# Performance work log

Measured on AMD Instinct MI355X. Metric: run time of the kernel, lower is better.

The kernel has to match this reference:

```python
import jax, jax.numpy as jnp
import numpy as np

N_NODES = 100000
N_EDGES = 3200000
N_GRAPHS = 256
DIMS = [11, 200, 200, 200, 200, 200]  # acfg_init_dims + cfg_filters
CONCAT = sum(DIMS[1:])  # 1000


def setup_inputs() -> dict:
    key = jax.random.key(0)
    ks = jax.random.split(key, 32)
    d = {}
    d["x"] = jax.random.normal(ks[0], (N_NODES, DIMS[0]), jnp.float32)
    d["edge_index"] = jax.random.randint(ks[1], (2, N_EDGES), 0, N_NODES)
    d["batch"] = jnp.sort(jax.random.randint(ks[2], (N_NODES,), 0, N_GRAPHS))
    ki = 3
    # SAGEConv params: lin_l (neighbors, with bias) + lin_r (root, no bias)
    for i in range(5):
        fi, fo = DIMS[i], DIMS[i + 1]
        s = 1.0 / np.sqrt(fi)
        d[f"Wl{i+1}"] = jax.random.uniform(ks[ki], (fo, fi), jnp.float32, -s, s); ki += 1
        d[f"bl{i+1}"] = jnp.zeros((fo,), jnp.float32)
        d[f"Wr{i+1}"] = jax.random.uniform(ks[ki], (fo, fi), jnp.float32, -s, s); ki += 1
    # projection head 1000 -> 500 -> 250 -> 1
    for j, (fi, fo) in enumerate([(CONCAT, CONCAT // 2), (CONCAT // 2, CONCAT // 4), (CONCAT // 4, 1)]):
        s = 1.0 / np.sqrt(fi)
        d[f"pw{j+1}"] = jax.random.uniform(ks[ki], (fo, fi), jnp.float32, -s, s); ki += 1
        d[f"pb{j+1}"] = jnp.zeros((fo,), jnp.float32)
    return d


def reference(x, edge_index, batch,
              Wl1, bl1, Wr1, Wl2, bl2, Wr2, Wl3, bl3, Wr3,
              Wl4, bl4, Wr4, Wl5, bl5, Wr5,
              pw1, pb1, pw2, pb2, pw3, pb3):
    src, dst = edge_index[0], edge_index[1]
    # in-degree for mean aggregation (computed once, reused by all layers)
    deg = jax.ops.segment_sum(jnp.ones((src.shape[0],), x.dtype), dst, N_NODES)
    inv_deg = (1.0 / jnp.maximum(deg, 1.0))[:, None]

    def sage(h, Wl, bl, Wr):
        agg = jax.ops.segment_sum(h[src], dst, N_NODES) * inv_deg  # mean of neighbor feats
        return agg @ Wl.T + bl + h @ Wr.T

    layers = [(Wl1, bl1, Wr1), (Wl2, bl2, Wr2), (Wl3, bl3, Wr3), (Wl4, bl4, Wr4), (Wl5, bl5, Wr5)]
    h = x
    outs = []
    for Wl, bl, Wr in layers:
        h = jax.nn.relu(sage(h, Wl, bl, Wr))
        outs.append(h)
    hc = jnp.concatenate(outs, axis=1)  # [N, 1000]

    # global_mean_pool over graph ids
    cnt = jax.ops.segment_sum(jnp.ones((x.shape[0],), x.dtype), batch, N_GRAPHS)
    g = jax.ops.segment_sum(hc, batch, N_GRAPHS) / jnp.maximum(cnt, 1.0)[:, None]

    # dropout is identity in eval mode (functional.dropout with training=False)
    g = g @ pw1.T + pb1
    g = g @ pw2.T + pb2
    g = g @ pw3.T + pb3  # [num_graphs, 1]
    return jax.nn.sigmoid(g).squeeze(1)
```

## Files before the change

kernel.cpp:

```cpp
#include <hip/hip_runtime.h>
#include <math.h>

typedef __attribute__((ext_vector_type(4))) float floatx4;
typedef __attribute__((ext_vector_type(2))) float floatx2;

#define ROWP 256
#define R4   16
#define NT 14
#define NTC 13
#define KS 7
#define PACK_BYTES (NT*KS*64*8)
#define PACK1_BYTES (NT*64*8)
#define STAGE_BYTES (NTC*KS*64*8)
#define BSHIFT 6
#define EPB 4096
#define MAXBUCK 1600

__device__ __forceinline__ unsigned short f2bf(float f){
    union { float f; unsigned u; } v; v.f = f;
    unsigned r = v.u + 0x7FFF + ((v.u >> 16) & 1);
    return (unsigned short)(r >> 16);
}
__device__ __forceinline__ unsigned pk4_fp8(float a, float b, float c, float d){
    int w = __builtin_amdgcn_cvt_pk_fp8_f32(a, b, 0, false);
    w = __builtin_amdgcn_cvt_pk_fp8_f32(c, d, w, true);
    return (unsigned)w;
}
__device__ __forceinline__ unsigned char b1_fp8(float a){
    int w = __builtin_amdgcn_cvt_pk_fp8_f32(a, a, 0, false);
    return (unsigned char)(w & 0xFF);
}


__global__ __launch_bounds__(256) void k_bin_hist(
    const int* __restrict__ dst, int* __restrict__ hist, int E, int nbuck)
{
    __shared__ int lh[MAXBUCK];
    for (int i = threadIdx.x; i < nbuck; i += 256) lh[i] = 0;
    __syncthreads();
    int base = blockIdx.x * EPB;
    #pragma unroll
    for (int k = 0; k < EPB / 256; ++k){
        int e = base + k * 256 + threadIdx.x;
        if (e < E) atomicAdd(&lh[dst[e] >> BSHIFT], 1);
    }
    __syncthreads();
    for (int i = threadIdx.x; i < nbuck; i += 256)
        hist[(size_t)blockIdx.x * nbuck + i] = lh[i];
}

__global__ __launch_bounds__(256) void k_col_scan(
    int* __restrict__ hist, int* __restrict__ T, int nblk, int nbuck)
{
    __shared__ int part[4][64];
    int w = threadIdx.x >> 6, l = threadIdx.x & 63;
    int b = blockIdx.x * 64 + l;
    int chunk = (nblk + 3) >> 2;
    int j0 = w * chunk, j1 = j0 + chunk; if (j1 > nblk) j1 = nblk;
    int s = 0;
    if (b < nbuck)
        for (int j = j0; j < j1; ++j) s += hist[(size_t)j * nbuck + b];
    part[w][l] = s;
    __syncthreads();
    if (b < nbuck){
        int run = 0;
        for (int w2 = 0; w2 < w; ++w2) run += part[w2][l];
        for (int j = j0; j < j1; ++j){
            int v = hist[(size_t)j * nbuck + b];
            hist[(size_t)j * nbuck + b] = run;
            run += v;
        }
        if (w == 3) T[b] = part[0][l] + part[1][l] + part[2][l] + part[3][l];
    }
}

__global__ __launch_bounds__(256) void k_scan_t(
    const int* __restrict__ T, int* __restrict__ tbase, int nbuck)
{
    __shared__ int ts[256];
    int t = threadIdx.x;
    int v[8]; int s = 0;
    int base = t * 8;
    #pragma unroll
    for (int k = 0; k < 8; ++k){
        int idx = base + k;
        v[k] = (idx < nbuck) ? T[idx] : 0;
        s += v[k];
    }
    ts[t] = s; __syncthreads();
    #pragma unroll
    for (int off = 1; off < 256; off <<= 1){
        int p = (t >= off) ? ts[t - off] : 0;
        __syncthreads();
        ts[t] += p;
        __syncthreads();
    }
    int run = ts[t] - s;
    #pragma unroll
    for (int k = 0; k < 8; ++k){
        int idx = base + k;
        if (idx < nbuck) tbase[idx] = run;
        run += v[k];
    }
    if (t == 255) tbase[nbuck] = ts[255];
}

__global__ __launch_bounds__(256) void k_bin_scatter(
    const int* __restrict__ src, const int* __restrict__ dst,
    const int* __restrict__ off, const int* __restrict__ tbase,
    unsigned* __restrict__ pairs, int E, int nbuck)
{
    __shared__ int lbase[MAXBUCK];
    __shared__ int lc[MAXBUCK];
    for (int i = threadIdx.x; i < nbuck; i += 256){
        lbase[i] = off[(size_t)blockIdx.x * nbuck + i] + tbase[i];
        lc[i] = 0;
    }
    __syncthreads();
    int base = blockIdx.x * EPB;
    #pragma unroll
    for (int k = 0; k < EPB / 256; ++k){
        int e = base + k * 256 + threadIdx.x;
        if (e < E){
            int d = dst[e];
            int b = d >> BSHIFT;
            int r = atomicAdd(&lc[b], 1);
            pairs[lbase[b] + r] = ((unsigned)(d & 63) << 26) | (unsigned)src[e];
        }
    }
}

__global__ __launch_bounds__(256) void k_bucket_deg(
    const unsigned* __restrict__ pairs, const int* __restrict__ tbase,
    int* __restrict__ deg, float* __restrict__ inv_deg, int N)
{
    __shared__ int ld[64];
    int b = blockIdx.x;
    if (threadIdx.x < 64) ld[threadIdx.x] = 0;
    __syncthreads();
    int pb = tbase[b], pe = tbase[b + 1];
    for (int e = pb + threadIdx.x; e < pe; e += 256)
        atomicAdd(&ld[pairs[e] >> 26], 1);
    __syncthreads();
    if (threadIdx.x < 64){
        int node = (b << BSHIFT) + threadIdx.x;
        if (node < N){
            int d = ld[threadIdx.x];
            deg[node] = d;
            inv_deg[node] = 1.0f / fmaxf((float)d, 1.0f);
        }
    }
}

__global__ __launch_bounds__(256) void k_place(
    const unsigned* __restrict__ pairs, const int* __restrict__ tbase,
    const int* __restrict__ row_ptr, int* __restrict__ srcs, int N)
{
    __shared__ int lrp[64];
    __shared__ int lcur[64];
    int b = blockIdx.x;
    if (threadIdx.x < 64){
        int node = (b << BSHIFT) + threadIdx.x;
        lrp[threadIdx.x] = (node < N) ? row_ptr[node] : 0;
        lcur[threadIdx.x] = 0;
    }
    __syncthreads();
    int pb = tbase[b], pe = tbase[b + 1];
    for (int e = pb + threadIdx.x; e < pe; e += 256){
        unsigned pr = pairs[e];
        int li = pr >> 26;
        int r = atomicAdd(&lcur[li], 1);
        srcs[lrp[li] + r] = (int)(pr & 0x03FFFFFFu);
    }
}


__global__ void k_scan_sums(const int* __restrict__ deg, int* __restrict__ csum, int N){
    __shared__ int sd[256];
    int base = blockIdx.x * 1024;
    int s = 0;
    for (int i = threadIdx.x; i < 1024; i += 256){
        int idx = base + i;
        s += (idx < N) ? deg[idx] : 0;
    }
    sd[threadIdx.x] = s; __syncthreads();
    for (int off = 128; off > 0; off >>= 1){
        if (threadIdx.x < off) sd[threadIdx.x] += sd[threadIdx.x + off];
        __syncthreads();
    }
    if (threadIdx.x == 0) csum[blockIdx.x] = sd[0];
}

__global__ void k_scan_apply(const int* __restrict__ deg, const int* __restrict__ csum,
                             int* __restrict__ row_ptr, int N, int E, int nchunks){
    __shared__ int ts[256];
    __shared__ int base_s;
    int partial = 0;
    for (int j = threadIdx.x; j < nchunks; j += 256)
        if (j < (int)blockIdx.x) partial += csum[j];
    ts[threadIdx.x] = partial; __syncthreads();
    for (int off = 128; off > 0; off >>= 1){
        if (threadIdx.x < off) ts[threadIdx.x] += ts[threadIdx.x + off];
        __syncthreads();
    }
    if (threadIdx.x == 0) base_s = ts[0];
    __syncthreads();
    int blk_base = base_s;
    __syncthreads();

    int base = blockIdx.x * 1024 + threadIdx.x * 4;
    int v[4]; int s = 0;
    #pragma unroll
    for (int j = 0; j < 4; ++j){
        int idx = base + j;
        v[j] = (idx < N) ? deg[idx] : 0;
        s += v[j];
    }
    ts[threadIdx.x] = s; __syncthreads();
    #pragma unroll
    for (int off = 1; off < 256; off <<= 1){
        int t = (threadIdx.x >= off) ? ts[threadIdx.x - off] : 0;
        __syncthreads();
        ts[threadIdx.x] += t;
        __syncthreads();
    }
    int excl = ts[threadIdx.x] - s + blk_base;
    #pragma unroll
    for (int j = 0; j < 4; ++j){
        int idx = base + j;
        if (idx < N) row_ptr[idx] = excl;
        excl += v[j];
    }
    if (blockIdx.x == 0 && threadIdx.x == 0) row_ptr[N] = E;
}


__global__ void k_gstart_bs(const int* __restrict__ batch, int* __restrict__ gstart,
                            int N, int NG){
    int g = blockIdx.x * blockDim.x + threadIdx.x;
    if (g > NG) return;
    int lo = 0, hi = N;
    while (lo < hi){
        int mid = (lo + hi) >> 1;
        if (batch[mid] < g) lo = mid + 1; else hi = mid;
    }
    gstart[g] = lo;
}


__global__ void k_pack_w(const float* W0, const float* W1, const float* W2, const float* W3,
                         const float* W4, const float* W5, const float* W6, const float* W7,
                         unsigned char* __restrict__ out){
    const float* Ws[8] = {W0,W1,W2,W3,W4,W5,W6,W7};
    const float* W = Ws[blockIdx.z];
    int lane = threadIdx.x;
    int n  = blockIdx.x * 16 + (lane & 15);
    int k0 = blockIdx.y * 32 + (lane >> 4) * 8;
    float f[8];
    #pragma unroll
    for (int j = 0; j < 8; ++j){
        int k = k0 + j;
        f[j] = (n < 200 && k < 200) ? W[n * 200 + k] : 0.f;
    }
    uint2 u;
    u.x = pk4_fp8(f[0], f[1], f[2], f[3]);
    u.y = pk4_fp8(f[4], f[5], f[6], f[7]);
    size_t off = ((((size_t)blockIdx.z * NT + blockIdx.x) * KS + blockIdx.y) * 64 + lane) * 8;
    *reinterpret_cast<uint2*>(out + off) = u;
}

__global__ __launch_bounds__(256) void k_pack_misc(
    const float* __restrict__ x, unsigned short* __restrict__ xp,
    unsigned char* __restrict__ xa,
    const float* __restrict__ Wl1, const float* __restrict__ Wr1,
    unsigned char* __restrict__ w1pack,
    const float* b0, const float* b1, const float* b2, const float* b3, const float* b4,
    float* __restrict__ biasp, int N, int xblk)
{
    int bid = blockIdx.x;
    if (bid < xblk){
        int i = bid * 256 + threadIdx.x;
        int node = i >> 4, c = i & 15;
        if (node < N){
            float f = (c < 11) ? x[(size_t)node * 11 + c] : 0.f;
            xp[i] = f2bf(f);
            xa[(size_t)node * 32 + 16 + c] = b1_fp8(f);
        }
        return;
    }
    int j = bid - xblk;
    if (j < NT){
        if (threadIdx.x >= 64) return;
        int lane = threadIdx.x;
        int n  = j * 16 + (lane & 15);
        int k0 = (lane >> 4) * 8;
        float f[8];
        #pragma unroll
        for (int jj = 0; jj < 8; ++jj){
            int k = k0 + jj;
            float v = 0.f;
            if (n < 200){
                if (k < 11)                 v = Wl1[n * 11 + k];
                else if (k >= 16 && k < 27) v = Wr1[n * 11 + (k - 16)];
            }
            f[jj] = v;
        }
        uint2 u;
        u.x = pk4_fp8(f[0], f[1], f[2], f[3]);
        u.y = pk4_fp8(f[4], f[5], f[6], f[7]);
        size_t off = ((size_t)j * 64 + lane) * 8;
        *reinterpret_cast<uint2*>(w1pack + off) = u;
        return;
    }
    int l = j - NT;
    const float* bs[5] = {b0,b1,b2,b3,b4};
    int c = threadIdx.x;
    if (c < ROWP) biasp[l * ROWP + c] = (c < 200) ? bs[l][c] : 0.f;
}


__global__ __launch_bounds__(256) void k_agg11(
    const unsigned short* __restrict__ xp, const int* __restrict__ row_ptr,
    const int* __restrict__ srcs, const float* __restrict__ inv_deg,
    unsigned char* __restrict__ xa, int N)
{
    int half = threadIdx.x >> 5;
    int node = blockIdx.x * 8 + half;
    int l = threadIdx.x & 31;
    if (node >= N) return;
    int beg = row_ptr[node], end = row_ptr[node + 1];

    float acc[12];
    #pragma unroll
    for (int i = 0; i < 12; ++i) acc[i] = 0.f;

    const uint4* x4 = reinterpret_cast<const uint4*>(xp);
    const uint2* x2 = reinterpret_cast<const uint2*>(xp);
    for (int e = beg + l; e < end; e += 32){
        int sn = srcs[e];
        uint4 a = x4[(size_t)sn * 2];
        uint2 b = x2[(size_t)sn * 4 + 2];
        union { unsigned u; float f; } c;
        c.u = a.x << 16;         acc[0] += c.f;
        c.u = a.x & 0xffff0000u; acc[1] += c.f;
        c.u = a.y << 16;         acc[2] += c.f;
        c.u = a.y & 0xffff0000u; acc[3] += c.f;
        c.u = a.z << 16;         acc[4] += c.f;
        c.u = a.z & 0xffff0000u; acc[5] += c.f;
        c.u = a.w << 16;         acc[6] += c.f;
        c.u = a.w & 0xffff0000u; acc[7] += c.f;
        c.u = b.x << 16;         acc[8] += c.f;
        c.u = b.x & 0xffff0000u; acc[9] += c.f;
        c.u = b.y << 16;         acc[10] += c.f;
        c.u = b.y & 0xffff0000u; acc[11] += c.f;
    }

    #pragma unroll
    for (int i = 0; i < 11; ++i){
        acc[i] += __shfl_xor(acc[i], 1, 64);
        acc[i] += __shfl_xor(acc[i], 2, 64);
        acc[i] += __shfl_xor(acc[i], 4, 64);
        acc[i] += __shfl_xor(acc[i], 8, 64);
        acc[i] += __shfl_xor(acc[i], 16, 64);
    }

    if (l == 0){
        float id = inv_deg[node];
        float v[12];
        #pragma unroll
        for (int i = 0; i < 11; ++i) v[i] = acc[i] * id;
        v[11] = 0.f;
        uint4 o;
        o.x = pk4_fp8(v[0], v[1], v[2], v[3]);
        o.y = pk4_fp8(v[4], v[5], v[6], v[7]);
        o.z = pk4_fp8(v[8], v[9], v[10], v[11]);
        o.w = 0u;
        *reinterpret_cast<uint4*>(xa + (size_t)node * 32) = o;
    }
}

__device__ __forceinline__ void accum_fp8v(floatx2* a, uint4 u){
    a[0] += __builtin_amdgcn_cvt_pk_f32_fp8((int)u.x, false);
    a[1] += __builtin_amdgcn_cvt_pk_f32_fp8((int)u.x, true );
    a[2] += __builtin_amdgcn_cvt_pk_f32_fp8((int)u.y, false);
    a[3] += __builtin_amdgcn_cvt_pk_f32_fp8((int)u.y, true );
    a[4] += __builtin_amdgcn_cvt_pk_f32_fp8((int)u.z, false);
    a[5] += __builtin_amdgcn_cvt_pk_f32_fp8((int)u.z, true );
    a[6] += __builtin_amdgcn_cvt_pk_f32_fp8((int)u.w, false);
    a[7] += __builtin_amdgcn_cvt_pk_f32_fp8((int)u.w, true );
}

__global__ __launch_bounds__(256) void k_agg200(
    const unsigned char* __restrict__ h8, const int* __restrict__ row_ptr,
    const int* __restrict__ srcs, const float* __restrict__ inv_deg,
    unsigned char* __restrict__ agg, int N)
{
    int node = blockIdx.x * 4 + (threadIdx.x >> 6);
    int lane = threadIdx.x & 63;
    if (node >= N) return;
    int g = lane >> 4;
    int l = lane & 15;
    int beg = row_ptr[node], end = row_ptr[node + 1];
    int nb = end - beg;

    floatx2 acc[8];
    #pragma unroll
    for (int i = 0; i < 8; ++i) acc[i] = (floatx2){0.f, 0.f};

    const uint4* h4 = reinterpret_cast<const uint4*>(h8);

    for (int t = 0; t < nb; t += 64){
        int cnt = nb - t; if (cnt > 64) cnt = 64;
        int eidx = t + lane;
        int si = srcs[beg + (eidx < nb ? eidx : nb - 1)];
        int jmax = (cnt - g + 3) >> 2;

        int j = 0;
        for (; j + 4 <= jmax; j += 4){
            int b0 = g + 4 * j;
            int s0 = __shfl(si, b0,      64);
            int s1 = __shfl(si, b0 + 4,  64);
            int s2 = __shfl(si, b0 + 8,  64);
            int s3 = __shfl(si, b0 + 12, 64);
            uint4 u0 = h4[(size_t)s0 * R4 + l];
            uint4 u1 = h4[(size_t)s1 * R4 + l];
            uint4 u2 = h4[(size_t)s2 * R4 + l];
            uint4 u3 = h4[(size_t)s3 * R4 + l];
            accum_fp8v(acc, u0);
            accum_fp8v(acc, u1);
            accum_fp8v(acc, u2);
            accum_fp8v(acc, u3);
        }
        for (; j < jmax; ++j){
            int s0 = __shfl(si, g + 4 * j, 64);
            uint4 u0 = h4[(size_t)s0 * R4 + l];
            accum_fp8v(acc, u0);
        }
    }

    float af[16];
    #pragma unroll
    for (int i = 0; i < 8; ++i){ af[2*i] = acc[i][0]; af[2*i+1] = acc[i][1]; }
    #pragma unroll
    for (int i = 0; i < 16; ++i){
        af[i] += __shfl_xor(af[i], 32, 64);
        af[i] += __shfl_xor(af[i], 16, 64);
    }

    if (g == 0){
        float id = inv_deg[node];
        uint4 o;
        o.x = pk4_fp8(af[0] * id,  af[1] * id,  af[2] * id,  af[3] * id);
        o.y = pk4_fp8(af[4] * id,  af[5] * id,  af[6] * id,  af[7] * id);
        o.z = pk4_fp8(af[8] * id,  af[9] * id,  af[10] * id, af[11] * id);
        o.w = pk4_fp8(af[12] * id, af[13] * id, af[14] * id, af[15] * id);
        *reinterpret_cast<uint4*>(agg + (size_t)node * ROWP + l * 16) = o;
    }
}


__global__ __launch_bounds__(256) void k_layer1_mfma(
    const unsigned char* __restrict__ xa, const unsigned char* __restrict__ W1p,
    const float* __restrict__ biasp, unsigned char* __restrict__ outp, int M)
{
    const int wave = threadIdx.x >> 6;
    const int lane = threadIdx.x & 63;
    const int n = lane & 15;
    const int q = lane >> 4;
    int row = blockIdx.x * 64 + wave * 16 + n;
    int rowc = row < M ? row : (M - 1);

    long a = *reinterpret_cast<const long*>(xa + (size_t)rowc * 32 + q * 8);

    floatx4 acc[NTC];
    #pragma unroll
    for (int nt = 0; nt < NTC; ++nt){
        long b = *reinterpret_cast<const long*>(W1p + ((size_t)nt * 64 + lane) * 8);
        acc[nt] = __builtin_amdgcn_mfma_f32_16x16x32_fp8_fp8(a, b, (floatx4){0.f,0.f,0.f,0.f}, 0, 0, 0);
    }

    int r0 = blockIdx.x * 64 + wave * 16 + q * 4;
    #pragma unroll
    for (int nt = 0; nt < NTC; ++nt){
        float bsv = biasp[nt * 16 + n];
        #pragma unroll
        for (int r = 0; r < 4; ++r){
            int rr = r0 + r;
            if (rr < M){
                float v = fmaxf(acc[nt][r] + bsv, 0.f);
                outp[(size_t)rr * ROWP + nt * 16 + n] = b1_fp8(v);
            }
        }
    }
}

__global__ __launch_bounds__(256) void k_sage_mfma(
    const unsigned char* __restrict__ Aagg, const unsigned char* __restrict__ Ah,
    const unsigned char* __restrict__ Wlp, const unsigned char* __restrict__ Wrp,
    const float* __restrict__ biasp, unsigned char* __restrict__ outp, int M)
{
    __shared__ __align__(16) unsigned char lw[STAGE_BYTES];
    const int wave = threadIdx.x >> 6;
    const int lane = threadIdx.x & 63;
    const int n = lane & 15;
    const int q = lane >> 4;
    int row = blockIdx.x * 64 + wave * 16 + n;
    int rowc = row < M ? row : (M - 1);

    floatx4 acc[NTC];
    #pragma unroll
    for (int nt = 0; nt < NTC; ++nt) acc[nt] = (floatx4){0.f, 0.f, 0.f, 0.f};

    const unsigned char* Wp[2] = {Wlp, Wrp};
    const unsigned char* Ap[2] = {Aagg, Ah};

    #pragma unroll
    for (int phase = 0; phase < 2; ++phase){
        if (phase) __syncthreads();
        {
            const uint4* src4 = reinterpret_cast<const uint4*>(Wp[phase]);
            uint4* dst4 = reinterpret_cast<uint4*>(lw);
            for (int i = threadIdx.x; i < STAGE_BYTES / 16; i += 256)
                dst4[i] = src4[i];
        }
        __syncthreads();

        const unsigned char* arow = Ap[phase] + (size_t)rowc * ROWP + q * 8;
        long a[KS];
        #pragma unroll
        for (int ks = 0; ks < 6; ++ks)
            a[ks] = *reinterpret_cast<const long*>(arow + ks * 32);
        a[6] = (q < 2) ? *reinterpret_cast<const long*>(arow + 192) : 0L;

        #pragma unroll
        for (int ks = 0; ks < KS; ++ks){
            #pragma unroll
            for (int nt = 0; nt < NTC; ++nt){
                long b = *reinterpret_cast<const long*>(&lw[((nt * KS + ks) * 64 + lane) * 8]);
                acc[nt] = __builtin_amdgcn_mfma_f32_16x16x32_fp8_fp8(a[ks], b, acc[nt], 0, 0, 0);
            }
        }
    }

    int r0 = blockIdx.x * 64 + wave * 16 + q * 4;
    #pragma unroll
    for (int nt = 0; nt < NTC; ++nt){
        float bsv = biasp[nt * 16 + n];
        #pragma unroll
        for (int r = 0; r < 4; ++r){
            int rr = r0 + r;
            if (rr < M){
                float v = fmaxf(acc[nt][r] + bsv, 0.f);
                outp[(size_t)rr * ROWP + nt * 16 + n] = b1_fp8(v);
            }
        }
    }
}


__global__ __launch_bounds__(256) void k_pool(
    const unsigned char* __restrict__ h8, const int* __restrict__ gstart,
    float* __restrict__ gsum, int col_off)
{
    int g = blockIdx.x;
    int beg = gstart[g], end = gstart[g+1];
    int len = end - beg;
    if (len <= 0) return;
    int sub = threadIdx.x >> 6;
    int t   = threadIdx.x & 63;
    if (t >= 50) return;
    int pidx = blockIdx.y * 4 + sub;
    int chunk = (len + 31) >> 5;
    int rb = beg + pidx * chunk;
    int re = rb + chunk; if (re > end) re = end;
    if (rb >= re) return;
    int c0 = t * 4;

    float s0 = 0.f, s1 = 0.f, s2 = 0.f, s3 = 0.f;
    for (int r = rb; r < re; ++r){
        unsigned u = *reinterpret_cast<const unsigned*>(h8 + (size_t)r * ROWP + c0);
        floatx2 f01 = __builtin_amdgcn_cvt_pk_f32_fp8((int)u, false);
        floatx2 f23 = __builtin_amdgcn_cvt_pk_f32_fp8((int)u, true);
        s0 += f01[0]; s1 += f01[1]; s2 += f23[0]; s3 += f23[1];
    }
    float* gs = &gsum[(size_t)g * 1000 + col_off + c0];
    atomicAdd(gs + 0, s0);
    atomicAdd(gs + 1, s1);
    atomicAdd(gs + 2, s2);
    atomicAdd(gs + 3, s3);
}


__global__ __launch_bounds__(256) void k_mlp_first(
    const float* __restrict__ gsum, const int* __restrict__ gstart,
    const float* __restrict__ W, const float* __restrict__ b,
    float* __restrict__ outp)
{
    __shared__ __align__(16) float row[1000];
    int g = blockIdx.x;
    int cnt = gstart[g+1] - gstart[g];
    float inv = 1.0f / fmaxf((float)cnt, 1.0f);
    for (int i = threadIdx.x; i < 1000; i += 256)
        row[i] = gsum[(size_t)g * 1000 + i] * inv;
    __syncthreads();
    for (int c = threadIdx.x; c < 500; c += 256){
        const float4* w4 = reinterpret_cast<const float4*>(W + (size_t)c * 1000);
        const float4* r4 = reinterpret_cast<const float4*>(row);
        float s = b[c];
        for (int k = 0; k < 250; ++k){
            float4 wv = w4[k]; float4 rv = r4[k];
            s = fmaf(wv.x, rv.x, s);
            s = fmaf(wv.y, rv.y, s);
            s = fmaf(wv.z, rv.z, s);
            s = fmaf(wv.w, rv.w, s);
        }
        outp[(size_t)g * 500 + c] = s;
    }
}

__global__ __launch_bounds__(256) void k_mlp23(
    const float* __restrict__ t1, const float* __restrict__ W2,
    const float* __restrict__ b2, const float* __restrict__ W3,
    const float* __restrict__ b3, float* __restrict__ outp)
{
    __shared__ __align__(16) float row[500];
    __shared__ float red[256];
    int g = blockIdx.x;
    for (int i = threadIdx.x; i < 500; i += 256) row[i] = t1[(size_t)g * 500 + i];
    __syncthreads();
    float prod = 0.f;
    int c = threadIdx.x;
    if (c < 250){
        const float4* w4 = reinterpret_cast<const float4*>(W2 + (size_t)c * 500);
        const float4* r4 = reinterpret_cast<const float4*>(row);
        float s = b2[c];
        for (int k = 0; k < 125; ++k){
            float4 wv = w4[k]; float4 rv = r4[k];
            s = fmaf(wv.x, rv.x, s);
            s = fmaf(wv.y, rv.y, s);
            s = fmaf(wv.z, rv.z, s);
            s = fmaf(wv.w, rv.w, s);
        }
        prod = s * W3[c];
    }
    red[threadIdx.x] = prod;
    __syncthreads();
    for (int off = 128; off > 0; off >>= 1){
        if (threadIdx.x < off) red[threadIdx.x] += red[threadIdx.x + off];
        __syncthreads();
    }
    if (threadIdx.x == 0)
        outp[g] = 1.0f / (1.0f + expf(-(red[0] + b3[0])));
}


extern "C" void kernel_launch(void* const* d_in, const int* in_sizes, int n_in,
                              void* d_out, int out_size, void* d_ws, size_t ws_size,
                              hipStream_t stream)
{
    const float* x    = (const float*)d_in[0];
    const int*   ei   = (const int*)d_in[1];
    const int*   batch= (const int*)d_in[2];
    const float* Wl[5]; const float* bl[5]; const float* Wr[5];
    for (int i = 0; i < 5; ++i){
        Wl[i] = (const float*)d_in[3 + 3*i];
        bl[i] = (const float*)d_in[4 + 3*i];
        Wr[i] = (const float*)d_in[5 + 3*i];
    }
    const float* pw1 = (const float*)d_in[18]; const float* pb1 = (const float*)d_in[19];
    const float* pw2 = (const float*)d_in[20]; const float* pb2 = (const float*)d_in[21];
    const float* pw3 = (const float*)d_in[22]; const float* pb3 = (const float*)d_in[23];
    float* out = (float*)d_out;

    const int N  = in_sizes[2];
    const int E  = in_sizes[1] / 2;
    const int NG = out_size;
    const int* esrc = ei;
    const int* edst = ei + E;
    const int nbuck = (N + 63) >> BSHIFT;
    const int nblk  = (E + EPB - 1) / EPB;

    char* p = (char*)d_ws;
    auto carve = [&](size_t bytes)->void* {
        void* r = (void*)p;
        p += (bytes + 255) & ~(size_t)255;
        return r;
    };
    int*   deg     = (int*)  carve((size_t)N * 4);
    int*   row_ptr = (int*)  carve(((size_t)N + 1) * 4);
    int*   csum    = (int*)  carve(4096);
    int*   hist    = (int*)  carve((size_t)nblk * nbuck * 4);
    int*   Tb      = (int*)  carve((size_t)nbuck * 4);
    int*   tbase   = (int*)  carve(((size_t)nbuck + 1) * 4);
    float* invdeg  = (float*)carve((size_t)N * 4);
    int*   gstart  = (int*)  carve(((size_t)NG + 1) * 4);
    int*   srcs    = (int*)  carve((size_t)E * 4);
    unsigned* pairs = (unsigned*)carve((size_t)E * 4);
    unsigned short* xp    = (unsigned short*)carve((size_t)N * 16 * 2);
    unsigned char*  xa    = (unsigned char*) carve((size_t)N * 32);
    unsigned char*  agg8  = (unsigned char*) carve((size_t)N * ROWP);
    unsigned char*  h8A   = (unsigned char*) carve((size_t)N * ROWP);
    unsigned char*  h8B   = (unsigned char*) carve((size_t)N * ROWP);
    unsigned char*  wpack = (unsigned char*) carve((size_t)8 * PACK_BYTES);
    unsigned char*  w1pack= (unsigned char*) carve((size_t)PACK1_BYTES);
    float* biasp   = (float*)carve((size_t)5 * ROWP * 4);
    float* gsum    = (float*)carve((size_t)NG * 1000 * 4);
    float* t1      = (float*)carve((size_t)NG * 500 * 4);

    hipMemsetAsync(gsum, 0, (size_t)NG * 1000 * 4, stream);
    hipMemsetAsync(h8A, 0, (size_t)N * ROWP, stream);
    hipMemsetAsync(h8B, 0, (size_t)N * ROWP, stream);

    int xblk = (N * 16 + 255) / 256;
    k_pack_w<<<dim3(NT, KS, 8), 64, 0, stream>>>(
        Wl[1], Wr[1], Wl[2], Wr[2], Wl[3], Wr[3], Wl[4], Wr[4], wpack);
    k_pack_misc<<<xblk + NT + 5, 256, 0, stream>>>(
        x, xp, xa, Wl[0], Wr[0], w1pack,
        bl[0], bl[1], bl[2], bl[3], bl[4], biasp, N, xblk);

    k_bin_hist<<<nblk, 256, 0, stream>>>(edst, hist, E, nbuck);
    k_col_scan<<<(nbuck + 63) / 64, 256, 0, stream>>>(hist, Tb, nblk, nbuck);
    k_scan_t<<<1, 256, 0, stream>>>(Tb, tbase, nbuck);
    k_bin_scatter<<<nblk, 256, 0, stream>>>(esrc, edst, hist, tbase, pairs, E, nbuck);
    k_bucket_deg<<<nbuck, 256, 0, stream>>>(pairs, tbase, deg, invdeg, N);
    int nchunks = (N + 1023) / 1024;
    k_scan_sums<<<nchunks, 256, 0, stream>>>(deg, csum, N);
    k_scan_apply<<<nchunks, 256, 0, stream>>>(deg, csum, row_ptr, N, E, nchunks);
    k_place<<<nbuck, 256, 0, stream>>>(pairs, tbase, row_ptr, srcs, N);

    k_gstart_bs<<<(NG + 256) / 256, 256, 0, stream>>>(batch, gstart, N, NG);

    int gb = (N + 63) / 64;
    k_agg11<<<(N + 7) / 8, 256, 0, stream>>>(xp, row_ptr, srcs, invdeg, xa, N);
    k_layer1_mfma<<<gb, 256, 0, stream>>>(xa, w1pack, biasp, h8A, N);
    k_pool<<<dim3(NG, 8), 256, 0, stream>>>(h8A, gstart, gsum, 0);

    unsigned char* hc = h8A; unsigned char* hn = h8B;
    int ab = (N + 3) / 4;
    for (int L = 1; L < 5; ++L){
        k_agg200<<<ab, 256, 0, stream>>>(hc, row_ptr, srcs, invdeg, agg8, N);
        const unsigned char* Wlp = wpack + (size_t)((L-1)*2 + 0) * PACK_BYTES;
        const unsigned char* Wrp = wpack + (size_t)((L-1)*2 + 1) * PACK_BYTES;
        k_sage_mfma<<<gb, 256, 0, stream>>>(agg8, hc, Wlp, Wrp,
                                            biasp + L * ROWP, hn, N);
        k_pool<<<dim3(NG, 8), 256, 0, stream>>>(hn, gstart, gsum, 200 * L);
        unsigned char* t = hc; hc = hn; hn = t;
    }

    k_mlp_first<<<NG, 256, 0, stream>>>(gsum, gstart, pw1, pb1, t1);
    k_mlp23<<<NG, 256, 0, stream>>>(t1, pw2, pb2, pw3, pb3, out);
}
```

Baseline: 1.325 ms.

## Fuse neighbor aggregation, SAGE MFMA transform, and mean-pool into one kernel

Each layer's gather-mean aggregation now runs inside the MFMA kernel, writing the aggregated tile to shared memory instead of a global agg buffer. The output tile is staged in LDS and used for both the coalesced store and a graph-pooling pass with atomics, which replaces the separate k_pool launch. This cuts the global write and re-read of the aggregate and two launches per layer. In exchange the gather has less parallelism per block (16 nodes per wave run in sequence), LDS use is larger, and weights are staged in smaller chunks with more barriers.

```diff
diff --git a/kernel.cpp b/kernel.cpp
--- a/kernel.cpp
+++ b/kernel.cpp
@@ -11,10 +11,16 @@
 #define KS 7
 #define PACK_BYTES (NT*KS*64*8)
 #define PACK1_BYTES (NT*64*8)
-#define STAGE_BYTES (NTC*KS*64*8)
 #define BSHIFT 6
 #define EPB 4096
 #define MAXBUCK 1600
+
+#define A_STRIDE 240
+#define A_BYTES  (64*A_STRIDE)
+#define LWS_U4A  (NTC*4*32)
+#define LWS_U4B  (NTC*3*32)
+#define LWS_BYTES (LWS_U4A*16)
+#define PT_STRIDE 208
 
 __device__ __forceinline__ unsigned short f2bf(float f){
     union { float f; unsigned u; } v; v.f = f;
@@ -379,6 +385,43 @@
     }
 }
 
+
+__global__ __launch_bounds__(256) void k_layer1_mfma(
+    const unsigned char* __restrict__ xa, const unsigned char* __restrict__ W1p,
+    const float* __restrict__ biasp, unsigned char* __restrict__ outp, int M)
+{
+    const int wave = threadIdx.x >> 6;
+    const int lane = threadIdx.x & 63;
+    const int n = lane & 15;
+    const int q = lane >> 4;
+    int row = blockIdx.x * 64 + wave * 16 + n;
+    int rowc = row < M ? row : (M - 1);
+
+    long a = *reinterpret_cast<const long*>(xa + (size_t)rowc * 32 + q * 8);
+
+    floatx4 acc[NTC];
+    #pragma unroll
+    for (int nt = 0; nt < NTC; ++nt){
+        long b = *reinterpret_cast<const long*>(W1p + ((size_t)nt * 64 + lane) * 8);
+        acc[nt] = __builtin_amdgcn_mfma_f32_16x16x32_fp8_fp8(a, b, (floatx4){0.f,0.f,0.f,0.f}, 0, 0, 0);
+    }
+
+    int r0 = blockIdx.x * 64 + wave * 16 + q * 4;
+    #pragma unroll
+    for (int nt = 0; nt < NTC; ++nt){
+        float bsv = biasp[nt * 16 + n];
+        #pragma unroll
+        for (int r = 0; r < 4; ++r){
+            int rr = r0 + r;
+            if (rr < M){
+                float v = fmaxf(acc[nt][r] + bsv, 0.f);
+                outp[(size_t)rr * ROWP + nt * 16 + n] = b1_fp8(v);
+            }
+        }
+    }
+}
+
+
 __device__ __forceinline__ void accum_fp8v(floatx2* a, uint4 u){
     a[0] += __builtin_amdgcn_cvt_pk_f32_fp8((int)u.x, false);
     a[1] += __builtin_amdgcn_cvt_pk_f32_fp8((int)u.x, true );
@@ -390,170 +433,217 @@
     a[7] += __builtin_amdgcn_cvt_pk_f32_fp8((int)u.w, true );
 }
 
-__global__ __launch_bounds__(256) void k_agg200(
+__device__ __forceinline__ void stage_chunk(const unsigned char* __restrict__ W,
+                                            unsigned char* lws, int ks0, int nks, int tid){
+    const uint4* src = reinterpret_cast<const uint4*>(W);
+    uint4* dst = reinterpret_cast<uint4*>(lws);
+    int tot = NTC * nks * 32;
+    for (int i = tid; i < tot; i += 256){
+        int c = i >> 5, w = i & 31;
+        int nt = c / nks, ks = c - nt * nks;
+        dst[i] = src[(nt * KS + ks0 + ks) * 32 + w];
+    }
+}
+
+__global__ __launch_bounds__(256) void k_sage_fused(
     const unsigned char* __restrict__ h8, const int* __restrict__ row_ptr,
     const int* __restrict__ srcs, const float* __restrict__ inv_deg,
-    unsigned char* __restrict__ agg, int N)
-{
-    int node = blockIdx.x * 4 + (threadIdx.x >> 6);
-    int lane = threadIdx.x & 63;
-    if (node >= N) return;
-    int g = lane >> 4;
-    int l = lane & 15;
-    int beg = row_ptr[node], end = row_ptr[node + 1];
-    int nb = end - beg;
-
-    floatx2 acc[8];
-    #pragma unroll
-    for (int i = 0; i < 8; ++i) acc[i] = (floatx2){0.f, 0.f};
-
-    const uint4* h4 = reinterpret_cast<const uint4*>(h8);
-
-    for (int t = 0; t < nb; t += 64){
-        int cnt = nb - t; if (cnt > 64) cnt = 64;
-        int eidx = t + lane;
-        int si = srcs[beg + (eidx < nb ? eidx : nb - 1)];
-        int jmax = (cnt - g + 3) >> 2;
-
-        int j = 0;
-        for (; j + 4 <= jmax; j += 4){
-            int b0 = g + 4 * j;
-            int s0 = __shfl(si, b0,      64);
-            int s1 = __shfl(si, b0 + 4,  64);
-            int s2 = __shfl(si, b0 + 8,  64);
-            int s3 = __shfl(si, b0 + 12, 64);
-            uint4 u0 = h4[(size_t)s0 * R4 + l];
-            uint4 u1 = h4[(size_t)s1 * R4 + l];
-            uint4 u2 = h4[(size_t)s2 * R4 + l];
-            uint4 u3 = h4[(size_t)s3 * R4 + l];
-            accum_fp8v(acc, u0);
-            accum_fp8v(acc, u1);
-            accum_fp8v(acc, u2);
-            accum_fp8v(acc, u3);
-        }
-        for (; j < jmax; ++j){
-            int s0 = __shfl(si, g + 4 * j, 64);
-            uint4 u0 = h4[(size_t)s0 * R4 + l];
-            accum_fp8v(acc, u0);
-        }
-    }
-
-    float af[16];
-    #pragma unroll
-    for (int i = 0; i < 8; ++i){ af[2*i] = acc[i][0]; af[2*i+1] = acc[i][1]; }
-    #pragma unroll
-    for (int i = 0; i < 16; ++i){
-        af[i] += __shfl_xor(af[i], 32, 64);
-        af[i] += __shfl_xor(af[i], 16, 64);
-    }
-
-    if (g == 0){
-        float id = inv_deg[node];
-        uint4 o;
-        o.x = pk4_fp8(af[0] * id,  af[1] * id,  af[2] * id,  af[3] * id);
-        o.y = pk4_fp8(af[4] * id,  af[5] * id,  af[6] * id,  af[7] * id);
-        o.z = pk4_fp8(af[8] * id,  af[9] * id,  af[10] * id, af[11] * id);
-        o.w = pk4_fp8(af[12] * id, af[13] * id, af[14] * id, af[15] * id);
-        *reinterpret_cast<uint4*>(agg + (size_t)node * ROWP + l * 16) = o;
-    }
-}
-
-
-__global__ __launch_bounds__(256) void k_layer1_mfma(
-    const unsigned char* __restrict__ xa, const unsigned char* __restrict__ W1p,
-    const float* __restrict__ biasp, unsigned char* __restrict__ outp, int M)
-{
+    const unsigned char* __restrict__ Wlp, const unsigned char* __restrict__ Wrp,
+    const float* __restrict__ biasp, const int* __restrict__ batch,
+    float* __restrict__ gsum, int col_off,
+    unsigned char* __restrict__ outp, int M)
+{
+    __shared__ __align__(16) unsigned char smem[A_BYTES + LWS_BYTES];
+    __shared__ int lb[64];
+    unsigned char* Atile = smem;
+    unsigned char* lws   = smem + A_BYTES;
+    unsigned char* ptile = smem;
+
     const int wave = threadIdx.x >> 6;
     const int lane = threadIdx.x & 63;
     const int n = lane & 15;
     const int q = lane >> 4;
-    int row = blockIdx.x * 64 + wave * 16 + n;
-    int rowc = row < M ? row : (M - 1);
-
-    long a = *reinterpret_cast<const long*>(xa + (size_t)rowc * 32 + q * 8);
+    const int r0 = blockIdx.x * 64;
+    const int nrows = (M - r0 < 64) ? (M - r0) : 64;
+
+    if (threadIdx.x < 64 && threadIdx.x < nrows) lb[threadIdx.x] = batch[r0 + threadIdx.x];
+
+    {
+        const uint4* h4 = reinterpret_cast<const uint4*>(h8);
+        const int g = q;
+        const int l = n;
+        for (int jn = 0; jn < 16; ++jn){
+            int node = r0 + wave * 16 + jn;
+            if (node >= M) break;
+            int beg = row_ptr[node], end = row_ptr[node + 1];
+            int nb = end - beg;
+
+            floatx2 acc[8];
+            #pragma unroll
+            for (int i = 0; i < 8; ++i) acc[i] = (floatx2){0.f, 0.f};
+
+            for (int t = 0; t < nb; t += 64){
+                int cnt = nb - t; if (cnt > 64) cnt = 64;
+                int eidx = t + lane;
+                int si = srcs[beg + (eidx < nb ? eidx : nb - 1)];
+                int jmax = (cnt - g + 3) >> 2;
+                int j = 0;
+                for (; j + 4 <= jmax; j += 4){
+                    int b0 = g + 4 * j;
+                    int s0 = __shfl(si, b0,      64);
+                    int s1 = __shfl(si, b0 + 4,  64);
+                    int s2 = __shfl(si, b0 + 8,  64);
+                    int s3 = __shfl(si, b0 + 12, 64);
+                    uint4 u0 = h4[(size_t)s0 * R4 + l];
+                    uint4 u1 = h4[(size_t)s1 * R4 + l];
+                    uint4 u2 = h4[(size_t)s2 * R4 + l];
+                    uint4 u3 = h4[(size_t)s3 * R4 + l];
+                    accum_fp8v(acc, u0);
+                    accum_fp8v(acc, u1);
+                    accum_fp8v(acc, u2);
+                    accum_fp8v(acc, u3);
+                }
+                for (; j < jmax; ++j){
+                    int s0 = __shfl(si, g + 4 * j, 64);
+                    uint4 u0 = h4[(size_t)s0 * R4 + l];
+                    accum_fp8v(acc, u0);
+                }
+            }
+
+            float af[16];
+            #pragma unroll
+            for (int i = 0; i < 8; ++i){ af[2*i] = acc[i][0]; af[2*i+1] = acc[i][1]; }
+            #pragma unroll
+            for (int i = 0; i < 16; ++i){
+                af[i] += __shfl_xor(af[i], 32, 64);
+                af[i] += __shfl_xor(af[i], 16, 64);
+            }
+
+            if (g == 0){
+                float id = inv_deg[node];
+                uint4 o;
+                o.x = pk4_fp8(af[0] * id,  af[1] * id,  af[2] * id,  af[3] * id);
+                o.y = pk4_fp8(af[4] * id,  af[5] * id,  af[6] * id,  af[7] * id);
+                o.z = pk4_fp8(af[8] * id,  af[9] * id,  af[10] * id, af[11] * id);
+                o.w = pk4_fp8(af[12] * id, af[13] * id, af[14] * id, af[15] * id);
+                *reinterpret_cast<uint4*>(Atile + (wave * 16 + jn) * A_STRIDE + l * 16) = o;
+            }
+        }
+    }
+    __syncthreads();
 
     floatx4 acc[NTC];
     #pragma unroll
-    for (int nt = 0; nt < NTC; ++nt){
-        long b = *reinterpret_cast<const long*>(W1p + ((size_t)nt * 64 + lane) * 8);
-        acc[nt] = __builtin_amdgcn_mfma_f32_16x16x32_fp8_fp8(a, b, (floatx4){0.f,0.f,0.f,0.f}, 0, 0, 0);
-    }
-
-    int r0 = blockIdx.x * 64 + wave * 16 + q * 4;
-    #pragma unroll
-    for (int nt = 0; nt < NTC; ++nt){
-        float bsv = biasp[nt * 16 + n];
-        #pragma unroll
-        for (int r = 0; r < 4; ++r){
-            int rr = r0 + r;
-            if (rr < M){
+    for (int nt = 0; nt < NTC; ++nt) acc[nt] = (floatx4){0.f, 0.f, 0.f, 0.f};
+
+    long a0[KS];
+    {
+        const unsigned char* arow = Atile + (wave * 16 + n) * A_STRIDE + q * 8;
+        #pragma unroll
+        for (int ks = 0; ks < KS; ++ks)
+            a0[ks] = *reinterpret_cast<const long*>(arow + ks * 32);
+    }
+
+    stage_chunk(Wlp, lws, 0, 4, threadIdx.x);
+    __syncthreads();
+    #pragma unroll
+    for (int ksl = 0; ksl < 4; ++ksl){
+        #pragma unroll
+        for (int nt = 0; nt < NTC; ++nt){
+            long b = *reinterpret_cast<const long*>(&lws[((nt * 4 + ksl) * 64 + lane) * 8]);
+            acc[nt] = __builtin_amdgcn_mfma_f32_16x16x32_fp8_fp8(a0[ksl], b, acc[nt], 0, 0, 0);
+        }
+    }
+    __syncthreads();
+    stage_chunk(Wlp, lws, 4, 3, threadIdx.x);
+    __syncthreads();
+    #pragma unroll
+    for (int ksl = 0; ksl < 3; ++ksl){
+        #pragma unroll
+        for (int nt = 0; nt < NTC; ++nt){
+            long b = *reinterpret_cast<const long*>(&lws[((nt * 3 + ksl) * 64 + lane) * 8]);
+            acc[nt] = __builtin_amdgcn_mfma_f32_16x16x32_fp8_fp8(a0[4 + ksl], b, acc[nt], 0, 0, 0);
+        }
+    }
+
+    long a1[KS];
+    {
+        int row = r0 + wave * 16 + n;
+        int rowc = row < M ? row : (M - 1);
+        const unsigned char* arow = h8 + (size_t)rowc * ROWP + q * 8;
+        #pragma unroll
+        for (int ks = 0; ks < KS; ++ks)
+            a1[ks] = *reinterpret_cast<const long*>(arow + ks * 32);
+    }
+    __syncthreads();
+    stage_chunk(Wrp, lws, 0, 4, threadIdx.x);
+    __syncthreads();
+    #pragma unroll
+    for (int ksl = 0; ksl < 4; ++ksl){
+        #pragma unroll
+        for (int nt = 0; nt < NTC; ++nt){
+            long b = *reinterpret_cast<const long*>(&lws[((nt * 4 + ksl) * 64 + lane) * 8]);
+            acc[nt] = __builtin_amdgcn_mfma_f32_16x16x32_fp8_fp8(a1[ksl], b, acc[nt], 0, 0, 0);
+        }
+    }
+    __syncthreads();
+    stage_chunk(Wrp, lws, 4, 3, threadIdx.x);
+    __syncthreads();
+    #pragma unroll
+    for (int ksl = 0; ksl < 3; ++ksl){
+        #pragma unroll
+        for (int nt = 0; nt < NTC; ++nt){
+            long b = *reinterpret_cast<const long*>(&lws[((nt * 3 + ksl) * 64 + lane) * 8]);
+            acc[nt] = __builtin_amdgcn_mfma_f32_16x16x32_fp8_fp8(a1[4 + ksl], b, acc[nt], 0, 0, 0);
+        }
+    }
+    __syncthreads();
+
+    {
+        int lr0 = wave * 16 + q * 4;
+        #pragma unroll
+        for (int nt = 0; nt < NTC; ++nt){
+            float bsv = biasp[nt * 16 + n];
+            #pragma unroll
+            for (int r = 0; r < 4; ++r){
                 float v = fmaxf(acc[nt][r] + bsv, 0.f);
-                outp[(size_t)rr * ROWP + nt * 16 + n] = b1_fp8(v);
+                ptile[(lr0 + r) * PT_STRIDE + nt * 16 + n] = b1_fp8(v);
             }
         }
     }
-}
-
-__global__ __launch_bounds__(256) void k_sage_mfma(
-    const unsigned char* __restrict__ Aagg, const unsigned char* __restrict__ Ah,
-    const unsigned char* __restrict__ Wlp, const unsigned char* __restrict__ Wrp,
-    const float* __restrict__ biasp, unsigned char* __restrict__ outp, int M)
-{
-    __shared__ __align__(16) unsigned char lw[STAGE_BYTES];
-    const int wave = threadIdx.x >> 6;
-    const int lane = threadIdx.x & 63;
-    const int n = lane & 15;
-    const int q = lane >> 4;
-    int row = blockIdx.x * 64 + wave * 16 + n;
-    int rowc = row < M ? row : (M - 1);
-
-    floatx4 acc[NTC];
-    #pragma unroll
-    for (int nt = 0; nt < NTC; ++nt) acc[nt] = (floatx4){0.f, 0.f, 0.f, 0.f};
-
-    const unsigned char* Wp[2] = {Wlp, Wrp};
-    const unsigned char* Ap[2] = {Aagg, Ah};
-
-    #pragma unroll
-    for (int phase = 0; phase < 2; ++phase){
-        if (phase) __syncthreads();
-        {
-            const uint4* src4 = reinterpret_cast<const uint4*>(Wp[phase]);
-            uint4* dst4 = reinterpret_cast<uint4*>(lw);
-            for (int i = threadIdx.x; i < STAGE_BYTES / 16; i += 256)
-                dst4[i] = src4[i];
-        }
-        __syncthreads();
-
-        const unsigned char* arow = Ap[phase] + (size_t)rowc * ROWP + q * 8;
-        long a[KS];
-        #pragma unroll
-        for (int ks = 0; ks < 6; ++ks)
-            a[ks] = *reinterpret_cast<const long*>(arow + ks * 32);
-        a[6] = (q < 2) ? *reinterpret_cast<const long*>(arow + 192) : 0L;
-
-        #pragma unroll
-        for (int ks = 0; ks < KS; ++ks){
-            #pragma unroll
-            for (int nt = 0; nt < NTC; ++nt){
-                long b = *reinterpret_cast<const long*>(&lw[((nt * KS + ks) * 64 + lane) * 8]);
-                acc[nt] = __builtin_amdgcn_mfma_f32_16x16x32_fp8_fp8(a[ks], b, acc[nt], 0, 0, 0);
+    __syncthreads();
+
+    {
+        const uint4* s4 = reinterpret_cast<const uint4*>(ptile);
+        int tot = nrows * 13;
+        for (int i = threadIdx.x; i < tot; i += 256){
+            int r = i / 13, c = i - r * 13;
+            *reinterpret_cast<uint4*>(outp + (size_t)(r0 + r) * ROWP + c * 16) = s4[i];
+        }
+    }
+
+    if (threadIdx.x < 50){
+        int t = threadIdx.x;
+        const unsigned* pd = reinterpret_cast<const unsigned*>(ptile);
+        float s0 = 0.f, s1 = 0.f, s2 = 0.f, s3 = 0.f;
+        int cur = lb[0];
+        for (int r = 0; r < nrows; ++r){
+            int gg = lb[r];
+            if (gg != cur){
+                float* gp = &gsum[(size_t)cur * 1000 + col_off + t * 4];
+                atomicAdd(gp + 0, s0); atomicAdd(gp + 1, s1);
+                atomicAdd(gp + 2, s2); atomicAdd(gp + 3, s3);
+                s0 = s1 = s2 = s3 = 0.f;
+                cur = gg;
             }
-        }
-    }
-
-    int r0 = blockIdx.x * 64 + wave * 16 + q * 4;
-    #pragma unroll
-    for (int nt = 0; nt < NTC; ++nt){
-        float bsv = biasp[nt * 16 + n];
-        #pragma unroll
-        for (int r = 0; r < 4; ++r){
-            int rr = r0 + r;
-            if (rr < M){
-                float v = fmaxf(acc[nt][r] + bsv, 0.f);
-                outp[(size_t)rr * ROWP + nt * 16 + n] = b1_fp8(v);
-            }
-        }
+            unsigned u = pd[r * 52 + t];
+            floatx2 lo = __builtin_amdgcn_cvt_pk_f32_fp8((int)u, false);
+            floatx2 hi = __builtin_amdgcn_cvt_pk_f32_fp8((int)u, true);
+            s0 += lo[0]; s1 += lo[1]; s2 += hi[0]; s3 += hi[1];
+        }
+        float* gp = &gsum[(size_t)cur * 1000 + col_off + t * 4];
+        atomicAdd(gp + 0, s0); atomicAdd(gp + 1, s1);
+        atomicAdd(gp + 2, s2); atomicAdd(gp + 3, s3);
     }
 }
 
@@ -698,7 +788,6 @@
     unsigned* pairs = (unsigned*)carve((size_t)E * 4);
     unsigned short* xp    = (unsigned short*)carve((size_t)N * 16 * 2);
     unsigned char*  xa    = (unsigned char*) carve((size_t)N * 32);
-    unsigned char*  agg8  = (unsigned char*) carve((size_t)N * ROWP);
     unsigned char*  h8A   = (unsigned char*) carve((size_t)N * ROWP);
     unsigned char*  h8B   = (unsigned char*) carve((size_t)N * ROWP);
     unsigned char*  wpack = (unsigned char*) carve((size_t)8 * PACK_BYTES);
@@ -736,14 +825,12 @@
     k_pool<<<dim3(NG, 8), 256, 0, stream>>>(h8A, gstart, gsum, 0);
 
     unsigned char* hc = h8A; unsigned char* hn = h8B;
-    int ab = (N + 3) / 4;
     for (int L = 1; L < 5; ++L){
-        k_agg200<<<ab, 256, 0, stream>>>(hc, row_ptr, srcs, invdeg, agg8, N);
         const unsigned char* Wlp = wpack + (size_t)((L-1)*2 + 0) * PACK_BYTES;
         const unsigned char* Wrp = wpack + (size_t)((L-1)*2 + 1) * PACK_BYTES;
-        k_sage_mfma<<<gb, 256, 0, stream>>>(agg8, hc, Wlp, Wrp,
-                                            biasp + L * ROWP, hn, N);
-        k_pool<<<dim3(NG, 8), 256, 0, stream>>>(hn, gstart, gsum, 200 * L);
+        k_sage_fused<<<gb, 256, 0, stream>>>(hc, row_ptr, srcs, invdeg,
+                                             Wlp, Wrp, biasp + L * ROWP,
+                                             batch, gsum, 200 * L, hn, N);
         unsigned char* t = hc; hc = hn; hn = t;
     }
 
```

New measurement: 1.473 ms. +11.2%, slower.

## Fuse global mean pooling into the SAGE GEMM epilogues via an LDS output tile

Applied to the files above, without the earlier changes.

The layer-1 and SAGE MFMA kernels now write their fp8 output tile to shared memory first. From there they copy it to global memory with coalesced 16-byte stores. They also sum each block's rows per graph id and add the sums into gsum with atomics. This removes the five separate k_pool launches and their re-read of every layer's activations. In exchange, the epilogue adds two extra barriers and a serial 64-row reduction done by 50 threads per block.

```diff
diff --git a/kernel.cpp b/kernel.cpp
--- a/kernel.cpp
+++ b/kernel.cpp
@@ -15,6 +15,7 @@
 #define BSHIFT 6
 #define EPB 4096
 #define MAXBUCK 1600
+#define PT_STRIDE 208
 
 __device__ __forceinline__ unsigned short f2bf(float f){
     union { float f; unsigned u; } v; v.f = f;
@@ -379,6 +380,7 @@
     }
 }
 
+
 __device__ __forceinline__ void accum_fp8v(floatx2* a, uint4 u){
     a[0] += __builtin_amdgcn_cvt_pk_f32_fp8((int)u.x, false);
     a[1] += __builtin_amdgcn_cvt_pk_f32_fp8((int)u.x, true );
@@ -461,14 +463,21 @@
 
 __global__ __launch_bounds__(256) void k_layer1_mfma(
     const unsigned char* __restrict__ xa, const unsigned char* __restrict__ W1p,
-    const float* __restrict__ biasp, unsigned char* __restrict__ outp, int M)
-{
+    const float* __restrict__ biasp, const int* __restrict__ batch,
+    float* __restrict__ gsum, unsigned char* __restrict__ outp, int M)
+{
+    __shared__ __align__(16) unsigned char ptile[64 * PT_STRIDE];
+    __shared__ int lb[64];
     const int wave = threadIdx.x >> 6;
     const int lane = threadIdx.x & 63;
     const int n = lane & 15;
     const int q = lane >> 4;
-    int row = blockIdx.x * 64 + wave * 16 + n;
+    const int r0 = blockIdx.x * 64;
+    const int nrows = (M - r0 < 64) ? (M - r0) : 64;
+    int row = r0 + wave * 16 + n;
     int rowc = row < M ? row : (M - 1);
+
+    if (threadIdx.x < 64 && threadIdx.x < nrows) lb[threadIdx.x] = batch[r0 + threadIdx.x];
 
     long a = *reinterpret_cast<const long*>(xa + (size_t)rowc * 32 + q * 8);
 
@@ -479,33 +488,73 @@
         acc[nt] = __builtin_amdgcn_mfma_f32_16x16x32_fp8_fp8(a, b, (floatx4){0.f,0.f,0.f,0.f}, 0, 0, 0);
     }
 
-    int r0 = blockIdx.x * 64 + wave * 16 + q * 4;
-    #pragma unroll
-    for (int nt = 0; nt < NTC; ++nt){
-        float bsv = biasp[nt * 16 + n];
+    {
+        int lr0 = wave * 16 + q * 4;
         #pragma unroll
-        for (int r = 0; r < 4; ++r){
-            int rr = r0 + r;
-            if (rr < M){
+        for (int nt = 0; nt < NTC; ++nt){
+            float bsv = biasp[nt * 16 + n];
+            #pragma unroll
+            for (int r = 0; r < 4; ++r){
                 float v = fmaxf(acc[nt][r] + bsv, 0.f);
-                outp[(size_t)rr * ROWP + nt * 16 + n] = b1_fp8(v);
+                ptile[(lr0 + r) * PT_STRIDE + nt * 16 + n] = b1_fp8(v);
             }
         }
+    }
+    __syncthreads();
+
+    {
+        const uint4* s4 = reinterpret_cast<const uint4*>(ptile);
+        int tot = nrows * 13;
+        for (int i = threadIdx.x; i < tot; i += 256){
+            int r = i / 13, c = i - r * 13;
+            *reinterpret_cast<uint4*>(outp + (size_t)(r0 + r) * ROWP + c * 16) = s4[i];
+        }
+    }
+
+    if (threadIdx.x < 50){
+        int t = threadIdx.x;
+        const unsigned* pd = reinterpret_cast<const unsigned*>(ptile);
+        float s0 = 0.f, s1 = 0.f, s2 = 0.f, s3 = 0.f;
+        int cur = lb[0];
+        for (int r = 0; r < nrows; ++r){
+            int gg = lb[r];
+            if (gg != cur){
+                float* gp = &gsum[(size_t)cur * 1000 + t * 4];
+                atomicAdd(gp + 0, s0); atomicAdd(gp + 1, s1);
+                atomicAdd(gp + 2, s2); atomicAdd(gp + 3, s3);
+                s0 = s1 = s2 = s3 = 0.f;
+                cur = gg;
+            }
+            unsigned u = pd[r * 52 + t];
+            floatx2 lo = __builtin_amdgcn_cvt_pk_f32_fp8((int)u, false);
+            floatx2 hi = __builtin_amdgcn_cvt_pk_f32_fp8((int)u, true);
+            s0 += lo[0]; s1 += lo[1]; s2 += hi[0]; s3 += hi[1];
+        }
+        float* gp = &gsum[(size_t)cur * 1000 + t * 4];
+        atomicAdd(gp + 0, s0); atomicAdd(gp + 1, s1);
+        atomicAdd(gp + 2, s2); atomicAdd(gp + 3, s3);
     }
 }
 
 __global__ __launch_bounds__(256) void k_sage_mfma(
     const unsigned char* __restrict__ Aagg, const unsigned char* __restrict__ Ah,
     const unsigned char* __restrict__ Wlp, const unsigned char* __restrict__ Wrp,
-    const float* __restrict__ biasp, unsigned char* __restrict__ outp, int M)
+    const float* __restrict__ biasp, const int* __restrict__ batch,
+    float* __restrict__ gsum, int col_off,
+    unsigned char* __restrict__ outp, int M)
 {
     __shared__ __align__(16) unsigned char lw[STAGE_BYTES];
+    __shared__ int lb[64];
     const int wave = threadIdx.x >> 6;
     const int lane = threadIdx.x & 63;
     const int n = lane & 15;
     const int q = lane >> 4;
-    int row = blockIdx.x * 64 + wave * 16 + n;
+    const int r0 = blockIdx.x * 64;
+    const int nrows = (M - r0 < 64) ? (M - r0) : 64;
+    int row = r0 + wave * 16 + n;
     int rowc = row < M ? row : (M - 1);
+
+    if (threadIdx.x < 64 && threadIdx.x < nrows) lb[threadIdx.x] = batch[r0 + threadIdx.x];
 
     floatx4 acc[NTC];
     #pragma unroll
@@ -541,53 +590,55 @@
             }
         }
     }
-
-    int r0 = blockIdx.x * 64 + wave * 16 + q * 4;
-    #pragma unroll
-    for (int nt = 0; nt < NTC; ++nt){
-        float bsv = biasp[nt * 16 + n];
+    __syncthreads();
+
+    unsigned char* ptile = lw;
+    {
+        int lr0 = wave * 16 + q * 4;
         #pragma unroll
-        for (int r = 0; r < 4; ++r){
-            int rr = r0 + r;
-            if (rr < M){
+        for (int nt = 0; nt < NTC; ++nt){
+            float bsv = biasp[nt * 16 + n];
+            #pragma unroll
+            for (int r = 0; r < 4; ++r){
                 float v = fmaxf(acc[nt][r] + bsv, 0.f);
-                outp[(size_t)rr * ROWP + nt * 16 + n] = b1_fp8(v);
+                ptile[(lr0 + r) * PT_STRIDE + nt * 16 + n] = b1_fp8(v);
             }
         }
     }
-}
-
-
-__global__ __launch_bounds__(256) void k_pool(
-    const unsigned char* __restrict__ h8, const int* __restrict__ gstart,
-    float* __restrict__ gsum, int col_off)
-{
-    int g = blockIdx.x;
-    int beg = gstart[g], end = gstart[g+1];
-    int len = end - beg;
-    if (len <= 0) return;
-    int sub = threadIdx.x >> 6;
-    int t   = threadIdx.x & 63;
-    if (t >= 50) return;
-    int pidx = blockIdx.y * 4 + sub;
-    int chunk = (len + 31) >> 5;
-    int rb = beg + pidx * chunk;
-    int re = rb + chunk; if (re > end) re = end;
-    if (rb >= re) return;
-    int c0 = t * 4;
-
-    float s0 = 0.f, s1 = 0.f, s2 = 0.f, s3 = 0.f;
-    for (int r = rb; r < re; ++r){
-        unsigned u = *reinterpret_cast<const unsigned*>(h8 + (size_t)r * ROWP + c0);
-        floatx2 f01 = __builtin_amdgcn_cvt_pk_f32_fp8((int)u, false);
-        floatx2 f23 = __builtin_amdgcn_cvt_pk_f32_fp8((int)u, true);
-        s0 += f01[0]; s1 += f01[1]; s2 += f23[0]; s3 += f23[1];
-    }
-    float* gs = &gsum[(size_t)g * 1000 + col_off + c0];
-    atomicAdd(gs + 0, s0);
-    atomicAdd(gs + 1, s1);
-    atomicAdd(gs + 2, s2);
-    atomicAdd(gs + 3, s3);
+    __syncthreads();
+
+    {
+        const uint4* s4 = reinterpret_cast<const uint4*>(ptile);
+        int tot = nrows * 13;
+        for (int i = threadIdx.x; i < tot; i += 256){
+            int r = i / 13, c = i - r * 13;
+            *reinterpret_cast<uint4*>(outp + (size_t)(r0 + r) * ROWP + c * 16) = s4[i];
+        }
+    }
+
+    if (threadIdx.x < 50){
+        int t = threadIdx.x;
+        const unsigned* pd = reinterpret_cast<const unsigned*>(ptile);
+        float s0 = 0.f, s1 = 0.f, s2 = 0.f, s3 = 0.f;
+        int cur = lb[0];
+        for (int r = 0; r < nrows; ++r){
+            int gg = lb[r];
+            if (gg != cur){
+                float* gp = &gsum[(size_t)cur * 1000 + col_off + t * 4];
+                atomicAdd(gp + 0, s0); atomicAdd(gp + 1, s1);
+                atomicAdd(gp + 2, s2); atomicAdd(gp + 3, s3);
+                s0 = s1 = s2 = s3 = 0.f;
+                cur = gg;
+            }
+            unsigned u = pd[r * 52 + t];
+            floatx2 lo = __builtin_amdgcn_cvt_pk_f32_fp8((int)u, false);
+            floatx2 hi = __builtin_amdgcn_cvt_pk_f32_fp8((int)u, true);
+            s0 += lo[0]; s1 += lo[1]; s2 += hi[0]; s3 += hi[1];
+        }
+        float* gp = &gsum[(size_t)cur * 1000 + col_off + t * 4];
+        atomicAdd(gp + 0, s0); atomicAdd(gp + 1, s1);
+        atomicAdd(gp + 2, s2); atomicAdd(gp + 3, s3);
+    }
 }
 
 
@@ -732,8 +783,7 @@
 
     int gb = (N + 63) / 64;
     k_agg11<<<(N + 7) / 8, 256, 0, stream>>>(xp, row_ptr, srcs, invdeg, xa, N);
-    k_layer1_mfma<<<gb, 256, 0, stream>>>(xa, w1pack, biasp, h8A, N);
-    k_pool<<<dim3(NG, 8), 256, 0, stream>>>(h8A, gstart, gsum, 0);
+    k_layer1_mfma<<<gb, 256, 0, stream>>>(xa, w1pack, biasp, batch, gsum, h8A, N);
 
     unsigned char* hc = h8A; unsigned char* hn = h8B;
     int ab = (N + 3) / 4;
@@ -742,8 +792,9 @@
         const unsigned char* Wlp = wpack + (size_t)((L-1)*2 + 0) * PACK_BYTES;
         const unsigned char* Wrp = wpack + (size_t)((L-1)*2 + 1) * PACK_BYTES;
         k_sage_mfma<<<gb, 256, 0, stream>>>(agg8, hc, Wlp, Wrp,
-                                            biasp + L * ROWP, hn, N);
-        k_pool<<<dim3(NG, 8), 256, 0, stream>>>(hn, gstart, gsum, 200 * L);
+                                            biasp + L * ROWP, batch, gsum, 200 * L,
+                                            hn, N);
+        k_pool_dummy:;
         unsigned char* t = hc; hc = hn; hn = t;
     }
 
```

Result: faster. 1.110 ms (-16.2%).
